# Kernel optimization log

Hardware: AMD Instinct MI355X
Metric: run time of the kernel (lower is better)

Reference implementation:

```python
import jax, jax.numpy as jnp
import numpy as np

Z, K, H, Y = 128, 256, 512, 4  # z_size, key_size, hidden_size, y_dim


def setup_inputs() -> dict:
    key = jax.random.key(0)
    ks = jax.random.split(key, 8)
    B, T, P = 512, 32, 32
    s = lambda k, shape, sc: (jax.random.normal(k, shape, jnp.float32) * sc)
    return {
        "x_seq": jax.random.normal(ks[0], (B, T, P, P), jnp.float32),
        "W_enc": s(ks[1], (P * P, Z), 0.03),
        "gamma": jnp.ones((Z,), jnp.float32),
        "beta": jnp.zeros((Z,), jnp.float32),
        "W_ih": s(ks[2], (4 * H, K + 1), 0.05),
        "W_hh": s(ks[3], (4 * H, H), 0.04),
        "b_ih": jnp.zeros((4 * H,), jnp.float32),
        "b_hh": jnp.zeros((4 * H,), jnp.float32),
        "W_key": s(ks[4], (K, H), 0.06),
        "b_key": jnp.zeros((K,), jnp.float32),
        "W_g": s(ks[5], (1, H), 0.06),
        "b_g": jnp.zeros((1,), jnp.float32),
        "conf_gain": jnp.ones((1,), jnp.float32),
        "conf_bias": jnp.zeros((1,), jnp.float32),
        "W_y": s(ks[6], (Y, H), 0.06),
        "b_y": jnp.zeros((Y,), jnp.float32),
    }


def _lstm_cell(x, h, c, W_ih, W_hh, b_ih, b_hh):
    # PyTorch gate order: i, f, g, o
    gates = x @ W_ih.T + b_ih + h @ W_hh.T + b_hh
    i, f, g, o = jnp.split(gates, 4, axis=-1)
    c = jax.nn.sigmoid(f) * c + jax.nn.sigmoid(i) * jnp.tanh(g)
    h = jax.nn.sigmoid(o) * jnp.tanh(c)
    return h, c


def _forward(x_seq, W_enc, gamma, beta, W_ih, W_hh, b_ih, b_hh,
             W_key, b_key, W_g, b_g, conf_gain, conf_bias, W_y, b_y):
    B, T, P, _ = x_seq.shape
    # encoder: flatten -> linear to z_size (stand-in for Encoder_mlp)
    z = x_seq.reshape(B, T, P * P) @ W_enc  # [B, T, Z]
    # context norm over the sequence dim (single task segment)
    mu = z.mean(axis=1, keepdims=True)
    sig = jnp.sqrt(z.var(axis=1, keepdims=True) + 1e-8)
    z = (z - mu) / sig * gamma + beta

    M = T + 1  # T+1 steps; final step feeds a zero z_t
    z_pad = jnp.concatenate([z, jnp.zeros((B, 1, Z), z.dtype)], axis=1)  # [B, M, Z]

    h0 = jnp.zeros((B, H), z.dtype)
    c0 = jnp.zeros((B, H), z.dtype)
    kr0 = jnp.zeros((B, K + 1), z.dtype)
    Mk0 = jnp.zeros((B, M, K), z.dtype)
    Mv0 = jnp.zeros((B, M, Z), z.dtype)

    def step(carry, t):
        h, c, key_r, M_k, M_v = carry
        z_t = jax.lax.dynamic_index_in_dim(z_pad, t, axis=1, keepdims=False)  # [B, Z]
        h, c = _lstm_cell(key_r, h, c, W_ih, W_hh, b_ih, b_hh)
        key_w = jax.nn.relu(h @ W_key.T + b_key)          # [B, K]
        g = jax.nn.sigmoid(h @ W_g.T + b_g)               # [B, 1]
        y_lin = h @ W_y.T + b_y                            # [B, Y]
        # attention read over valid memory slots j < t
        scores = jnp.einsum('bz,bmz->bm', z_t, M_v)        # [B, M]
        valid = (jnp.arange(M) < t)[None, :]
        w_k = jax.nn.softmax(jnp.where(valid, scores, -1e9), axis=1)
        c_k = jax.nn.sigmoid(scores * conf_gain + conf_bias)
        kv = jnp.concatenate([M_k, c_k[..., None]], axis=2)  # [B, M, K+1]
        attn = g * jnp.einsum('bm,bmd->bd', w_k, kv)          # [B, K+1]
        key_r_new = jnp.where(t == 0, jnp.zeros_like(attn), attn)
        # append to memory at slot t
        M_k = jax.lax.dynamic_update_slice_in_dim(M_k, key_w[:, None, :], t, axis=1)
        M_v = jax.lax.dynamic_update_slice_in_dim(M_v, z_t[:, None, :], t, axis=1)
        return (h, c, key_r_new, M_k, M_v), y_lin

    _, ys = jax.lax.scan(step, (h0, c0, kr0, Mk0, Mv0), jnp.arange(M))
    return ys[-1]  # y_pred_linear from final step, [B, Y]


def reference(x_seq, W_enc, gamma, beta, W_ih, W_hh, b_ih, b_hh,
              W_key, b_key, W_g, b_g, conf_gain, conf_bias, W_y, b_y):
    y_pred_linear = _forward(x_seq, W_enc, gamma, beta, W_ih, W_hh, b_ih, b_hh,
                             W_key, b_key, W_g, b_g, conf_gain, conf_bias, W_y, b_y)
    y_pred = jnp.argmax(y_pred_linear, axis=1)
    return y_pred_linear, y_pred
```

## Files before the change

kernel.cpp:

```cpp
#include <hip/hip_runtime.h>
#include <math.h>

typedef unsigned short ushort;
typedef unsigned int uint;
typedef __bf16 bf16x8 __attribute__((ext_vector_type(8)));
typedef float f32x4 __attribute__((ext_vector_type(4)));

#define ZS    128
#define KS    256
#define HS    512
#define BATCH 512
#define TT    32
#define MM    33
#define NB    2304
#define KPAD  800
#define HOFF  272
#define LDA   800

static __device__ __forceinline__ float sigf(float x) { return 1.f / (1.f + expf(-x)); }

__global__ void prep_w(const float* __restrict__ W_ih, const float* __restrict__ W_hh,
                       const float* __restrict__ W_key, const float* __restrict__ b_ih,
                       const float* __restrict__ b_hh, const float* __restrict__ b_key,
                       const float* __restrict__ W_enc,
                       ushort* __restrict__ Whi, ushort* __restrict__ Wlo,
                       ushort* __restrict__ Behi, ushort* __restrict__ Belo,
                       float* __restrict__ biasN)
{
    int idx = blockIdx.x * 256 + threadIdx.x;
    if (idx < NB) {
        float bv;
        if (idx < 2048) { int j = idx >> 2, gi = idx & 3, r = gi * 512 + j; bv = b_ih[r] + b_hh[r]; }
        else bv = b_key[idx - 2048];
        biasN[idx] = bv;
    }
    if (idx < NB * KPAD) {
        int n = idx / KPAD, k = idx - n * KPAD;
        float v = 0.f;
        if (n < 2048) {
            int j = n >> 2, gi = n & 3, r = gi * 512 + j;
            if (k < 257) v = W_ih[r * 257 + k];
            else if (k >= HOFF && k < HOFF + 512) v = W_hh[r * 512 + (k - HOFF)];
        } else {
            if (k >= HOFF && k < HOFF + 512) v = W_key[(n - 2048) * 512 + (k - HOFF)];
        }
        uint u = __float_as_uint(v);
        Whi[idx] = (ushort)(u >> 16);
        float lo = v - __uint_as_float(u & 0xFFFF0000u);
        Wlo[idx] = (ushort)(__float_as_uint(lo) >> 16);
    } else if (idx < NB * KPAD + 128 * 1024) {
        int e = idx - NB * KPAD;
        int n = e >> 10, k = e & 1023;
        float v = W_enc[k * 128 + n];
        uint u = __float_as_uint(v);
        Behi[e] = (ushort)(u >> 16);
        float lo = v - __uint_as_float(u & 0xFFFF0000u);
        Belo[e] = (ushort)(__float_as_uint(lo) >> 16);
    }
}

template<int BN, int MODE>
__global__ __launch_bounds__(256)
void gemm_mfma(const float* __restrict__ A, int lda,
               const ushort* __restrict__ Bhi, const ushort* __restrict__ Blo, int ldb,
               int nslice,
               float* __restrict__ out, const float* __restrict__ biasN,
               float* __restrict__ cst, float* __restrict__ Mk, int step)
{
    constexpr int NI = BN / 32;
    constexpr int AHI = 0, ALO = 2560, BHI = 5120, BLO = 5120 + 40 * BN;
    constexpr int BUF = 5120 + 80 * BN;
    __shared__ ushort lds[2 * BUF];

    const int tid = threadIdx.x;
    const int bx = blockIdx.x, by = blockIdx.y;
    const int row0 = by * 64, n0 = bx * BN;
    const int l = tid & 63, w = tid >> 6, wm = w >> 1, wn = w & 1;
    const int lm = l & 15, kg = (l >> 4) << 3;

    f32x4 acc[2][NI];
    const f32x4 zero4 = {0.f, 0.f, 0.f, 0.f};
#pragma unroll
    for (int mi = 0; mi < 2; mi++)
#pragma unroll
        for (int ni = 0; ni < NI; ni++) acc[mi][ni] = zero4;

    float4 av[2];
    uint4 bhv[BN / 64], blv[BN / 64];

    auto LOADG = [&](int s) {
        const int k0 = s * 32;
#pragma unroll
        for (int i = 0; i < 2; i++) {
            int idx = tid + 256 * i, r = idx >> 3, c = (idx & 7) << 2;
            av[i] = *(const float4*)(A + (size_t)(row0 + r) * lda + k0 + c);
        }
#pragma unroll
        for (int i = 0; i < BN / 64; i++) {
            int idx = tid + 256 * i, r = idx >> 2, c = (idx & 3) << 3;
            bhv[i] = *(const uint4*)(Bhi + (size_t)(n0 + r) * ldb + k0 + c);
            blv[i] = *(const uint4*)(Blo + (size_t)(n0 + r) * ldb + k0 + c);
        }
    };
    auto STORE = [&](int buf) {
        ushort* L = lds + buf * BUF;
#pragma unroll
        for (int i = 0; i < 2; i++) {
            int idx = tid + 256 * i, r = idx >> 3, c = (idx & 7) << 2;
            uint u0 = __float_as_uint(av[i].x), u1 = __float_as_uint(av[i].y);
            uint u2 = __float_as_uint(av[i].z), u3 = __float_as_uint(av[i].w);
            uint hp0 = (u1 & 0xFFFF0000u) | (u0 >> 16);
            uint hp1 = (u3 & 0xFFFF0000u) | (u2 >> 16);
            float l0 = av[i].x - __uint_as_float(u0 & 0xFFFF0000u);
            float l1 = av[i].y - __uint_as_float(u1 & 0xFFFF0000u);
            float l2 = av[i].z - __uint_as_float(u2 & 0xFFFF0000u);
            float l3 = av[i].w - __uint_as_float(u3 & 0xFFFF0000u);
            uint lp0 = (__float_as_uint(l1) & 0xFFFF0000u) | (__float_as_uint(l0) >> 16);
            uint lp1 = (__float_as_uint(l3) & 0xFFFF0000u) | (__float_as_uint(l2) >> 16);
            *(uint2*)&L[AHI + r * 40 + c] = make_uint2(hp0, hp1);
            *(uint2*)&L[ALO + r * 40 + c] = make_uint2(lp0, lp1);
        }
#pragma unroll
        for (int i = 0; i < BN / 64; i++) {
            int idx = tid + 256 * i, r = idx >> 2, c = (idx & 3) << 3;
            *(uint4*)&L[BHI + r * 40 + c] = bhv[i];
            *(uint4*)&L[BLO + r * 40 + c] = blv[i];
        }
    };

    LOADG(0);
    STORE(0);
    for (int s = 0; s < nslice; s++) {
        if (s + 1 < nslice) LOADG(s + 1);
        __syncthreads();
        const ushort* L = lds + (s & 1) * BUF;
        bf16x8 ah[2], alv[2], bh[NI], bl[NI];
#pragma unroll
        for (int mi = 0; mi < 2; mi++) {
            int r = wm * 32 + mi * 16 + lm;
            ah[mi]  = *(const bf16x8*)&L[AHI + r * 40 + kg];
            alv[mi] = *(const bf16x8*)&L[ALO + r * 40 + kg];
        }
#pragma unroll
        for (int ni = 0; ni < NI; ni++) {
            int r = wn * (BN / 2) + ni * 16 + lm;
            bh[ni] = *(const bf16x8*)&L[BHI + r * 40 + kg];
            bl[ni] = *(const bf16x8*)&L[BLO + r * 40 + kg];
        }
#pragma unroll
        for (int mi = 0; mi < 2; mi++)
#pragma unroll
            for (int ni = 0; ni < NI; ni++) {
                acc[mi][ni] = __builtin_amdgcn_mfma_f32_16x16x32_bf16(ah[mi],  bh[ni], acc[mi][ni], 0, 0, 0);
                acc[mi][ni] = __builtin_amdgcn_mfma_f32_16x16x32_bf16(ah[mi],  bl[ni], acc[mi][ni], 0, 0, 0);
                acc[mi][ni] = __builtin_amdgcn_mfma_f32_16x16x32_bf16(alv[mi], bh[ni], acc[mi][ni], 0, 0, 0);
            }
        if (s + 1 < nslice) STORE((s + 1) & 1);
    }

    const int crow = (l >> 4) << 2;
    if (MODE == 0) {
#pragma unroll
        for (int mi = 0; mi < 2; mi++)
#pragma unroll
            for (int ni = 0; ni < NI; ni++)
#pragma unroll
                for (int r = 0; r < 4; r++) {
                    int m = row0 + wm * 32 + mi * 16 + crow + r;
                    int z = n0 + wn * (BN / 2) + ni * 16 + lm;
                    out[(size_t)(m >> 5) * (MM * ZS) + (m & 31) * ZS + z] = acc[mi][ni][r];
                }
    } else if (bx < 32) {
        __syncthreads();
        float* epi = (float*)lds;
        float* ew = epi + w * 1088;
#pragma unroll
        for (int mi = 0; mi < 2; mi++)
#pragma unroll
            for (int ni = 0; ni < NI; ni++)
#pragma unroll
                for (int r = 0; r < 4; r++) {
                    int ml = mi * 16 + crow + r, nl = ni * 16 + lm;
                    ew[ml * 34 + nl] = acc[mi][ni][r] + biasN[n0 + wn * 32 + nl];
                }
        __syncthreads();
        int bl_ = tid >> 2, ug = tid & 3;
        int b = row0 + bl_;
        int j0 = bx * 16 + ug * 4;
        float4 cold = *(float4*)&cst[(size_t)b * HS + j0];
        float cc[4] = {cold.x, cold.y, cold.z, cold.w};
        float hv[4];
#pragma unroll
        for (int i = 0; i < 4; i++) {
            int ul = ug * 4 + i;
            float p[4];
#pragma unroll
            for (int g = 0; g < 4; g++) {
                int nb = ul * 4 + g;
                p[g] = epi[((bl_ >> 5) * 2 + (nb >> 5)) * 1088 + (bl_ & 31) * 34 + (nb & 31)];
            }
            float ig = sigf(p[0]), fg = sigf(p[1]), gg = tanhf(p[2]), og = sigf(p[3]);
            float cn = fg * cc[i] + ig * gg;
            hv[i] = og * tanhf(cn);
            cc[i] = cn;
        }
        *(float4*)&cst[(size_t)b * HS + j0] = make_float4(cc[0], cc[1], cc[2], cc[3]);
        *(float4*)&out[(size_t)b * LDA + HOFF + j0] = make_float4(hv[0], hv[1], hv[2], hv[3]);
    } else if (step >= 1) {
#pragma unroll
        for (int mi = 0; mi < 2; mi++)
#pragma unroll
            for (int ni = 0; ni < NI; ni++)
#pragma unroll
                for (int r = 0; r < 4; r++) {
                    int b = row0 + wm * 32 + mi * 16 + crow + r;
                    int cg = n0 + wn * 32 + ni * 16 + lm;
                    float v = fmaxf(acc[mi][ni][r] + biasN[cg], 0.f);
                    Mk[((size_t)(step - 1) * BATCH + b) * KS + (cg - 2048)] = v;
                }
    }
}

__global__ void norm_k(float* __restrict__ z_pad, const float* __restrict__ gamma,
                       const float* __restrict__ beta)
{
    int b = blockIdx.x, zc = threadIdx.x;
    float* zb = z_pad + (size_t)b * (MM * ZS);
    float s = 0.f, s2 = 0.f;
    for (int t = 0; t < TT; t++) { float v = zb[t * ZS + zc]; s += v; s2 += v * v; }
    float mu = s * (1.f / 32.f);
    float var = s2 * (1.f / 32.f) - mu * mu;
    float rstd = 1.f / sqrtf(var + 1e-8f);
    float ga = gamma[zc], be = beta[zc];
    for (int t = 0; t < TT; t++) {
        float v = zb[t * ZS + zc];
        zb[t * ZS + zc] = (v - mu) * rstd * ga + be;
    }
    zb[TT * ZS + zc] = 0.f;
}

__global__ __launch_bounds__(256)
void scores_k(const float* __restrict__ z_pad, const float* __restrict__ cg_p,
              const float* __restrict__ cb_p, float* __restrict__ watt,
              float* __restrict__ wc)
{
    __shared__ float zs[MM * 129];
    int b = blockIdx.x, tid = threadIdx.x;
    const float* zb = z_pad + (size_t)b * (MM * ZS);
    for (int i = tid; i < MM * ZS; i += 256) {
        int m = i >> 7, k = i & 127;
        zs[m * 129 + k] = zb[i];
    }
    __syncthreads();
    float cg = cg_p[0], cb = cb_p[0];
    int wid = tid >> 6, lane = tid & 63;
    for (int t = 1 + wid; t <= 32; t += 4) {
        int m = lane;
        float s = -3.0e38f;
        if (m < t) {
            const float* zt = &zs[t * 129];
            const float* zm = &zs[m * 129];
            float acc = 0.f;
#pragma unroll 8
            for (int k = 0; k < ZS; k++) acc += zt[k] * zm[k];
            s = acc;
        }
        float mx = s;
        for (int off = 1; off < 64; off <<= 1) mx = fmaxf(mx, __shfl_xor(mx, off));
        float e = (m < t) ? expf(s - mx) : 0.f;
        float sum = e;
        for (int off = 1; off < 64; off <<= 1) sum += __shfl_xor(sum, off);
        float w = e / sum;
        if (m < t) watt[(b * MM + t) * MM + m] = w;
        float p = (m < t) ? w * sigf(s * cg + cb) : 0.f;
        for (int off = 1; off < 64; off <<= 1) p += __shfl_xor(p, off);
        if (lane == 0) wc[b * MM + t] = p;
    }
}

__global__ __launch_bounds__(256)
void post_k(float* __restrict__ inpN, const float* __restrict__ W_g,
            const float* __restrict__ b_g, const float* __restrict__ watt,
            const float* __restrict__ wc, const float* __restrict__ Mk, int t)
{
    __shared__ float red[256];
    __shared__ float wts[32];
    __shared__ float gsh;
    int b = blockIdx.x, tid = threadIdx.x;
    float* row = inpN + (size_t)b * LDA;
    float h1 = row[HOFF + tid], h2 = row[HOFF + 256 + tid];
    red[tid] = h1 * W_g[tid] + h2 * W_g[tid + 256];
    if (tid < t) wts[tid] = watt[(b * MM + t) * MM + tid];
    __syncthreads();
    for (int s = 128; s > 0; s >>= 1) {
        if (tid < s) red[tid] += red[tid + s];
        __syncthreads();
    }
    if (tid == 0) gsh = sigf(red[0] + b_g[0]);
    __syncthreads();
    float g = gsh;
    float acc = 0.f;
    for (int m = 0; m < t; m++)
        acc += wts[m] * Mk[((size_t)m * BATCH + b) * KS + tid];
    row[tid] = g * acc;
    if (tid == 0) row[256] = g * wc[b * MM + t];
}

__global__ void y_k(const float* __restrict__ inpN, const float* __restrict__ W_y,
                    const float* __restrict__ b_y, float* __restrict__ out)
{
    int b = blockIdx.x, lane = threadIdx.x;
    const float* h = inpN + (size_t)b * LDA + HOFF;
    float a0 = 0, a1 = 0, a2 = 0, a3 = 0;
    for (int r = 0; r < 8; r++) {
        int k = lane + r * 64;
        float hv = h[k];
        a0 += hv * W_y[k];
        a1 += hv * W_y[512 + k];
        a2 += hv * W_y[1024 + k];
        a3 += hv * W_y[1536 + k];
    }
    for (int off = 32; off > 0; off >>= 1) {
        a0 += __shfl_xor(a0, off);
        a1 += __shfl_xor(a1, off);
        a2 += __shfl_xor(a2, off);
        a3 += __shfl_xor(a3, off);
    }
    if (lane == 0) {
        float y0 = a0 + b_y[0], y1 = a1 + b_y[1], y2 = a2 + b_y[2], y3 = a3 + b_y[3];
        out[b * 4 + 0] = y0; out[b * 4 + 1] = y1; out[b * 4 + 2] = y2; out[b * 4 + 3] = y3;
        int best = 0; float bv = y0;
        if (y1 > bv) { bv = y1; best = 1; }
        if (y2 > bv) { bv = y2; best = 2; }
        if (y3 > bv) { bv = y3; best = 3; }
        out[2048 + b] = (float)best;
    }
}

extern "C" void kernel_launch(void* const* d_in, const int* in_sizes, int n_in,
                              void* d_out, int out_size, void* d_ws, size_t ws_size,
                              hipStream_t stream)
{
    const float* x_seq = (const float*)d_in[0];
    const float* W_enc = (const float*)d_in[1];
    const float* gamma = (const float*)d_in[2];
    const float* beta  = (const float*)d_in[3];
    const float* W_ih  = (const float*)d_in[4];
    const float* W_hh  = (const float*)d_in[5];
    const float* b_ih  = (const float*)d_in[6];
    const float* b_hh  = (const float*)d_in[7];
    const float* W_key = (const float*)d_in[8];
    const float* b_key = (const float*)d_in[9];
    const float* W_g   = (const float*)d_in[10];
    const float* b_g   = (const float*)d_in[11];
    const float* cgain = (const float*)d_in[12];
    const float* cbias = (const float*)d_in[13];
    const float* W_y   = (const float*)d_in[14];
    const float* b_y   = (const float*)d_in[15];

    float* ws    = (float*)d_ws;
    float* z_pad = ws;
    float* watt  = z_pad + 2162688;
    float* wcv   = watt + 557568;
    float* Mk    = wcv + 16896;
    float* inp0  = Mk + 4194304;
    float* inp1  = inp0 + 409600;
    float* cst   = inp1 + 409600;
    float* biasN = cst + 262144;
    ushort* Whi  = (ushort*)(biasN + 2304);
    ushort* Wlo  = Whi + NB * KPAD;
    ushort* Behi = Wlo + NB * KPAD;
    ushort* Belo = Behi + 131072;

    hipMemsetAsync(inp0, 0, (size_t)(409600 * 2 + 262144) * sizeof(float), stream);

    prep_w<<<(NB * KPAD + 131072 + 255) / 256, 256, 0, stream>>>(
        W_ih, W_hh, W_key, b_ih, b_hh, b_key, W_enc, Whi, Wlo, Behi, Belo, biasN);

    gemm_mfma<128, 0><<<dim3(1, 256), 256, 0, stream>>>(
        x_seq, 1024, Behi, Belo, 1024, 32, z_pad, nullptr, nullptr, nullptr, 0);
    norm_k<<<512, 128, 0, stream>>>(z_pad, gamma, beta);
    scores_k<<<512, 256, 0, stream>>>(z_pad, cgain, cbias, watt, wcv);

    for (int t = 0; t <= 32; t++) {
        float* inC = (t & 1) ? inp1 : inp0;
        float* inN = (t & 1) ? inp0 : inp1;
        gemm_mfma<64, 1><<<dim3(36, 8), 256, 0, stream>>>(
            inC, LDA, Whi, Wlo, KPAD, 25, inN, biasN, cst, Mk, t);
        if (t >= 1 && t <= 31)
            post_k<<<512, 256, 0, stream>>>(inN, W_g, b_g, watt, wcv, Mk, t);
    }
    y_k<<<512, 64, 0, stream>>>(inp1, W_y, b_y, (float*)d_out);
}
```

Measured before the change: 1.140 ms.

## Halve GEMM row tile and store recurrent activations pre-split as bf16 hi/lo

The GEMM row tile shrinks from 64 to 32 rows and a min-blocks launch bound is added, doubling the grid of the per-step LSTM GEMM (36x16) and the encoder GEMM (1x512) so more CUs are occupied. The recurrent input buffers are now stored as pre-split bf16 hi/lo pairs, written by the GEMM epilogue and post_k, so the per-step GEMM loads ready-made bf16 A tiles and skips the fp32 split arithmetic in its staging path. This trades more reloading of B tiles across row blocks and an extra split in the epilogues for less per-step A conversion and better parallelism.

```diff
diff --git a/kernel.cpp b/kernel.cpp
--- a/kernel.cpp
+++ b/kernel.cpp
@@ -18,6 +18,7 @@
 #define LDA   800
 
 static __device__ __forceinline__ float sigf(float x) { return 1.f / (1.f + expf(-x)); }
+static __device__ __forceinline__ float bf2f(ushort u) { return __uint_as_float((uint)u << 16); }
 
 __global__ void prep_w(const float* __restrict__ W_ih, const float* __restrict__ W_hh,
                        const float* __restrict__ W_key, const float* __restrict__ b_ih,
@@ -59,41 +60,46 @@
     }
 }
 
-template<int BN, int MODE>
-__global__ __launch_bounds__(256)
-void gemm_mfma(const float* __restrict__ A, int lda,
+template<int BN, int MODE, bool PRESPLIT>
+__global__ __launch_bounds__(256, 4)
+void gemm_mfma(const float* __restrict__ A,
+               const ushort* __restrict__ Ahi, const ushort* __restrict__ Alo, int lda,
                const ushort* __restrict__ Bhi, const ushort* __restrict__ Blo, int ldb,
                int nslice,
-               float* __restrict__ out, const float* __restrict__ biasN,
+               float* __restrict__ out,
+               ushort* __restrict__ outHi, ushort* __restrict__ outLo,
+               const float* __restrict__ biasN,
                float* __restrict__ cst, float* __restrict__ Mk, int step)
 {
     constexpr int NI = BN / 32;
-    constexpr int AHI = 0, ALO = 2560, BHI = 5120, BLO = 5120 + 40 * BN;
-    constexpr int BUF = 5120 + 80 * BN;
+    constexpr int AHI = 0, ALO = 32 * 40, BHI = 64 * 40, BLO = 64 * 40 + BN * 40;
+    constexpr int BUF = 64 * 40 + 2 * BN * 40;
     __shared__ ushort lds[2 * BUF];
 
     const int tid = threadIdx.x;
     const int bx = blockIdx.x, by = blockIdx.y;
-    const int row0 = by * 64, n0 = bx * BN;
+    const int row0 = by * 32, n0 = bx * BN;
     const int l = tid & 63, w = tid >> 6, wm = w >> 1, wn = w & 1;
     const int lm = l & 15, kg = (l >> 4) << 3;
 
-    f32x4 acc[2][NI];
+    f32x4 acc[NI];
     const f32x4 zero4 = {0.f, 0.f, 0.f, 0.f};
 #pragma unroll
-    for (int mi = 0; mi < 2; mi++)
-#pragma unroll
-        for (int ni = 0; ni < NI; ni++) acc[mi][ni] = zero4;
-
-    float4 av[2];
+    for (int ni = 0; ni < NI; ni++) acc[ni] = zero4;
+
+    float4 avf;
+    uint4 avu;
     uint4 bhv[BN / 64], blv[BN / 64];
 
     auto LOADG = [&](int s) {
         const int k0 = s * 32;
-#pragma unroll
-        for (int i = 0; i < 2; i++) {
-            int idx = tid + 256 * i, r = idx >> 3, c = (idx & 7) << 2;
-            av[i] = *(const float4*)(A + (size_t)(row0 + r) * lda + k0 + c);
+        if (PRESPLIT) {
+            int idx = tid & 127, r = idx >> 2, c = (idx & 3) << 3;
+            const ushort* src = (tid < 128) ? Ahi : Alo;
+            avu = *(const uint4*)(src + (size_t)(row0 + r) * lda + k0 + c);
+        } else {
+            int r = tid >> 3, c = (tid & 7) << 2;
+            avf = *(const float4*)(A + (size_t)(row0 + r) * lda + k0 + c);
         }
 #pragma unroll
         for (int i = 0; i < BN / 64; i++) {
@@ -104,17 +110,19 @@
     };
     auto STORE = [&](int buf) {
         ushort* L = lds + buf * BUF;
-#pragma unroll
-        for (int i = 0; i < 2; i++) {
-            int idx = tid + 256 * i, r = idx >> 3, c = (idx & 7) << 2;
-            uint u0 = __float_as_uint(av[i].x), u1 = __float_as_uint(av[i].y);
-            uint u2 = __float_as_uint(av[i].z), u3 = __float_as_uint(av[i].w);
+        if (PRESPLIT) {
+            int idx = tid & 127, r = idx >> 2, c = (idx & 3) << 3;
+            *(uint4*)&L[(tid < 128 ? AHI : ALO) + r * 40 + c] = avu;
+        } else {
+            int r = tid >> 3, c = (tid & 7) << 2;
+            uint u0 = __float_as_uint(avf.x), u1 = __float_as_uint(avf.y);
+            uint u2 = __float_as_uint(avf.z), u3 = __float_as_uint(avf.w);
             uint hp0 = (u1 & 0xFFFF0000u) | (u0 >> 16);
             uint hp1 = (u3 & 0xFFFF0000u) | (u2 >> 16);
-            float l0 = av[i].x - __uint_as_float(u0 & 0xFFFF0000u);
-            float l1 = av[i].y - __uint_as_float(u1 & 0xFFFF0000u);
-            float l2 = av[i].z - __uint_as_float(u2 & 0xFFFF0000u);
-            float l3 = av[i].w - __uint_as_float(u3 & 0xFFFF0000u);
+            float l0 = avf.x - __uint_as_float(u0 & 0xFFFF0000u);
+            float l1 = avf.y - __uint_as_float(u1 & 0xFFFF0000u);
+            float l2 = avf.z - __uint_as_float(u2 & 0xFFFF0000u);
+            float l3 = avf.w - __uint_as_float(u3 & 0xFFFF0000u);
             uint lp0 = (__float_as_uint(l1) & 0xFFFF0000u) | (__float_as_uint(l0) >> 16);
             uint lp1 = (__float_as_uint(l3) & 0xFFFF0000u) | (__float_as_uint(l2) >> 16);
             *(uint2*)&L[AHI + r * 40 + c] = make_uint2(hp0, hp1);
@@ -134,12 +142,11 @@
         if (s + 1 < nslice) LOADG(s + 1);
         __syncthreads();
         const ushort* L = lds + (s & 1) * BUF;
-        bf16x8 ah[2], alv[2], bh[NI], bl[NI];
-#pragma unroll
-        for (int mi = 0; mi < 2; mi++) {
-            int r = wm * 32 + mi * 16 + lm;
-            ah[mi]  = *(const bf16x8*)&L[AHI + r * 40 + kg];
-            alv[mi] = *(const bf16x8*)&L[ALO + r * 40 + kg];
+        bf16x8 ah, alv, bh[NI], bl[NI];
+        {
+            int r = wm * 16 + lm;
+            ah  = *(const bf16x8*)&L[AHI + r * 40 + kg];
+            alv = *(const bf16x8*)&L[ALO + r * 40 + kg];
         }
 #pragma unroll
         for (int ni = 0; ni < NI; ni++) {
@@ -148,76 +155,74 @@
             bl[ni] = *(const bf16x8*)&L[BLO + r * 40 + kg];
         }
 #pragma unroll
-        for (int mi = 0; mi < 2; mi++)
-#pragma unroll
-            for (int ni = 0; ni < NI; ni++) {
-                acc[mi][ni] = __builtin_amdgcn_mfma_f32_16x16x32_bf16(ah[mi],  bh[ni], acc[mi][ni], 0, 0, 0);
-                acc[mi][ni] = __builtin_amdgcn_mfma_f32_16x16x32_bf16(ah[mi],  bl[ni], acc[mi][ni], 0, 0, 0);
-                acc[mi][ni] = __builtin_amdgcn_mfma_f32_16x16x32_bf16(alv[mi], bh[ni], acc[mi][ni], 0, 0, 0);
-            }
+        for (int ni = 0; ni < NI; ni++) {
+            acc[ni] = __builtin_amdgcn_mfma_f32_16x16x32_bf16(ah,  bh[ni], acc[ni], 0, 0, 0);
+            acc[ni] = __builtin_amdgcn_mfma_f32_16x16x32_bf16(ah,  bl[ni], acc[ni], 0, 0, 0);
+            acc[ni] = __builtin_amdgcn_mfma_f32_16x16x32_bf16(alv, bh[ni], acc[ni], 0, 0, 0);
+        }
         if (s + 1 < nslice) STORE((s + 1) & 1);
     }
 
     const int crow = (l >> 4) << 2;
     if (MODE == 0) {
 #pragma unroll
-        for (int mi = 0; mi < 2; mi++)
-#pragma unroll
-            for (int ni = 0; ni < NI; ni++)
-#pragma unroll
-                for (int r = 0; r < 4; r++) {
-                    int m = row0 + wm * 32 + mi * 16 + crow + r;
-                    int z = n0 + wn * (BN / 2) + ni * 16 + lm;
-                    out[(size_t)(m >> 5) * (MM * ZS) + (m & 31) * ZS + z] = acc[mi][ni][r];
-                }
+        for (int ni = 0; ni < NI; ni++)
+#pragma unroll
+            for (int r = 0; r < 4; r++) {
+                int m = row0 + wm * 16 + crow + r;
+                int z = n0 + wn * (BN / 2) + ni * 16 + lm;
+                out[(size_t)(m >> 5) * (MM * ZS) + (m & 31) * ZS + z] = acc[ni][r];
+            }
     } else if (bx < 32) {
         __syncthreads();
         float* epi = (float*)lds;
-        float* ew = epi + w * 1088;
-#pragma unroll
-        for (int mi = 0; mi < 2; mi++)
-#pragma unroll
-            for (int ni = 0; ni < NI; ni++)
-#pragma unroll
-                for (int r = 0; r < 4; r++) {
-                    int ml = mi * 16 + crow + r, nl = ni * 16 + lm;
-                    ew[ml * 34 + nl] = acc[mi][ni][r] + biasN[n0 + wn * 32 + nl];
-                }
+        float* ew = epi + w * 544;
+#pragma unroll
+        for (int ni = 0; ni < NI; ni++)
+#pragma unroll
+            for (int r = 0; r < 4; r++) {
+                int ml = crow + r, nl = ni * 16 + lm;
+                ew[ml * 34 + nl] = acc[ni][r] + biasN[n0 + wn * 32 + nl];
+            }
         __syncthreads();
-        int bl_ = tid >> 2, ug = tid & 3;
-        int b = row0 + bl_;
-        int j0 = bx * 16 + ug * 4;
-        float4 cold = *(float4*)&cst[(size_t)b * HS + j0];
-        float cc[4] = {cold.x, cold.y, cold.z, cold.w};
-        float hv[4];
-#pragma unroll
-        for (int i = 0; i < 4; i++) {
-            int ul = ug * 4 + i;
+        int row = tid >> 3, jj8 = tid & 7;
+        int b = row0 + row;
+        int j0 = bx * 16 + jj8 * 2;
+        float2 cold = *(float2*)&cst[(size_t)b * HS + j0];
+        float cc[2] = {cold.x, cold.y}, hv[2];
+#pragma unroll
+        for (int i = 0; i < 2; i++) {
+            int jj = jj8 * 2 + i;
             float p[4];
 #pragma unroll
             for (int g = 0; g < 4; g++) {
-                int nb = ul * 4 + g;
-                p[g] = epi[((bl_ >> 5) * 2 + (nb >> 5)) * 1088 + (bl_ & 31) * 34 + (nb & 31)];
+                int n = jj * 4 + g;
+                int wv = (row >> 4) * 2 + (n >> 5);
+                p[g] = epi[wv * 544 + (row & 15) * 34 + (n & 31)];
             }
             float ig = sigf(p[0]), fg = sigf(p[1]), gg = tanhf(p[2]), og = sigf(p[3]);
             float cn = fg * cc[i] + ig * gg;
             hv[i] = og * tanhf(cn);
             cc[i] = cn;
         }
-        *(float4*)&cst[(size_t)b * HS + j0] = make_float4(cc[0], cc[1], cc[2], cc[3]);
-        *(float4*)&out[(size_t)b * LDA + HOFF + j0] = make_float4(hv[0], hv[1], hv[2], hv[3]);
+        *(float2*)&cst[(size_t)b * HS + j0] = make_float2(cc[0], cc[1]);
+        uint u0 = __float_as_uint(hv[0]), u1 = __float_as_uint(hv[1]);
+        uint hp = (u1 & 0xFFFF0000u) | (u0 >> 16);
+        float l0 = hv[0] - __uint_as_float(u0 & 0xFFFF0000u);
+        float l1 = hv[1] - __uint_as_float(u1 & 0xFFFF0000u);
+        uint lp = (__float_as_uint(l1) & 0xFFFF0000u) | (__float_as_uint(l0) >> 16);
+        *(uint*)&outHi[(size_t)b * LDA + HOFF + j0] = hp;
+        *(uint*)&outLo[(size_t)b * LDA + HOFF + j0] = lp;
     } else if (step >= 1) {
 #pragma unroll
-        for (int mi = 0; mi < 2; mi++)
-#pragma unroll
-            for (int ni = 0; ni < NI; ni++)
-#pragma unroll
-                for (int r = 0; r < 4; r++) {
-                    int b = row0 + wm * 32 + mi * 16 + crow + r;
-                    int cg = n0 + wn * 32 + ni * 16 + lm;
-                    float v = fmaxf(acc[mi][ni][r] + biasN[cg], 0.f);
-                    Mk[((size_t)(step - 1) * BATCH + b) * KS + (cg - 2048)] = v;
-                }
+        for (int ni = 0; ni < NI; ni++)
+#pragma unroll
+            for (int r = 0; r < 4; r++) {
+                int b = row0 + wm * 16 + crow + r;
+                int cg = n0 + wn * 32 + ni * 16 + lm;
+                float v = fmaxf(acc[ni][r] + biasN[cg], 0.f);
+                Mk[((size_t)(step - 1) * BATCH + b) * KS + (cg - 2048)] = v;
+            }
     }
 }
 
@@ -279,16 +284,19 @@
 }
 
 __global__ __launch_bounds__(256)
-void post_k(float* __restrict__ inpN, const float* __restrict__ W_g,
-            const float* __restrict__ b_g, const float* __restrict__ watt,
-            const float* __restrict__ wc, const float* __restrict__ Mk, int t)
+void post_k(ushort* __restrict__ inpHi, ushort* __restrict__ inpLo,
+            const float* __restrict__ W_g, const float* __restrict__ b_g,
+            const float* __restrict__ watt, const float* __restrict__ wc,
+            const float* __restrict__ Mk, int t)
 {
     __shared__ float red[256];
     __shared__ float wts[32];
     __shared__ float gsh;
     int b = blockIdx.x, tid = threadIdx.x;
-    float* row = inpN + (size_t)b * LDA;
-    float h1 = row[HOFF + tid], h2 = row[HOFF + 256 + tid];
+    ushort* rHi = inpHi + (size_t)b * LDA;
+    ushort* rLo = inpLo + (size_t)b * LDA;
+    float h1 = bf2f(rHi[HOFF + tid]) + bf2f(rLo[HOFF + tid]);
+    float h2 = bf2f(rHi[HOFF + 256 + tid]) + bf2f(rLo[HOFF + 256 + tid]);
     red[tid] = h1 * W_g[tid] + h2 * W_g[tid + 256];
     if (tid < t) wts[tid] = watt[(b * MM + t) * MM + tid];
     __syncthreads();
@@ -302,19 +310,31 @@
     float acc = 0.f;
     for (int m = 0; m < t; m++)
         acc += wts[m] * Mk[((size_t)m * BATCH + b) * KS + tid];
-    row[tid] = g * acc;
-    if (tid == 0) row[256] = g * wc[b * MM + t];
-}
-
-__global__ void y_k(const float* __restrict__ inpN, const float* __restrict__ W_y,
-                    const float* __restrict__ b_y, float* __restrict__ out)
+    float v = g * acc;
+    uint u = __float_as_uint(v);
+    rHi[tid] = (ushort)(u >> 16);
+    float lo = v - __uint_as_float(u & 0xFFFF0000u);
+    rLo[tid] = (ushort)(__float_as_uint(lo) >> 16);
+    if (tid == 0) {
+        float vc = g * wc[b * MM + t];
+        uint uc = __float_as_uint(vc);
+        rHi[256] = (ushort)(uc >> 16);
+        float lc = vc - __uint_as_float(uc & 0xFFFF0000u);
+        rLo[256] = (ushort)(__float_as_uint(lc) >> 16);
+    }
+}
+
+__global__ void y_k(const ushort* __restrict__ inpHi, const ushort* __restrict__ inpLo,
+                    const float* __restrict__ W_y, const float* __restrict__ b_y,
+                    float* __restrict__ out)
 {
     int b = blockIdx.x, lane = threadIdx.x;
-    const float* h = inpN + (size_t)b * LDA + HOFF;
+    const ushort* hHi = inpHi + (size_t)b * LDA + HOFF;
+    const ushort* hLo = inpLo + (size_t)b * LDA + HOFF;
     float a0 = 0, a1 = 0, a2 = 0, a3 = 0;
     for (int r = 0; r < 8; r++) {
         int k = lane + r * 64;
-        float hv = h[k];
+        float hv = bf2f(hHi[k]) + bf2f(hLo[k]);
         a0 += hv * W_y[k];
         a1 += hv * W_y[512 + k];
         a2 += hv * W_y[1024 + k];
@@ -363,32 +383,39 @@
     float* watt  = z_pad + 2162688;
     float* wcv   = watt + 557568;
     float* Mk    = wcv + 16896;
-    float* inp0  = Mk + 4194304;
-    float* inp1  = inp0 + 409600;
-    float* cst   = inp1 + 409600;
-    float* biasN = cst + 262144;
-    ushort* Whi  = (ushort*)(biasN + 2304);
+    float* biasN = Mk + 4194304;
+    float* cst   = biasN + 2304;
+    ushort* inpHi0 = (ushort*)(cst + 262144);
+    ushort* inpLo0 = inpHi0 + 409600;
+    ushort* inpHi1 = inpLo0 + 409600;
+    ushort* inpLo1 = inpHi1 + 409600;
+    ushort* Whi  = inpLo1 + 409600;
     ushort* Wlo  = Whi + NB * KPAD;
     ushort* Behi = Wlo + NB * KPAD;
     ushort* Belo = Behi + 131072;
 
-    hipMemsetAsync(inp0, 0, (size_t)(409600 * 2 + 262144) * sizeof(float), stream);
+    hipMemsetAsync(cst, 0, 262144 * sizeof(float) + 4 * 409600 * sizeof(ushort), stream);
 
     prep_w<<<(NB * KPAD + 131072 + 255) / 256, 256, 0, stream>>>(
         W_ih, W_hh, W_key, b_ih, b_hh, b_key, W_enc, Whi, Wlo, Behi, Belo, biasN);
 
-    gemm_mfma<128, 0><<<dim3(1, 256), 256, 0, stream>>>(
-        x_seq, 1024, Behi, Belo, 1024, 32, z_pad, nullptr, nullptr, nullptr, 0);
+    gemm_mfma<128, 0, false><<<dim3(1, 512), 256, 0, stream>>>(
+        x_seq, nullptr, nullptr, 1024, Behi, Belo, 1024, 32,
+        z_pad, nullptr, nullptr, nullptr, nullptr, nullptr, 0);
     norm_k<<<512, 128, 0, stream>>>(z_pad, gamma, beta);
     scores_k<<<512, 256, 0, stream>>>(z_pad, cgain, cbias, watt, wcv);
 
     for (int t = 0; t <= 32; t++) {
-        float* inC = (t & 1) ? inp1 : inp0;
-        float* inN = (t & 1) ? inp0 : inp1;
-        gemm_mfma<64, 1><<<dim3(36, 8), 256, 0, stream>>>(
-            inC, LDA, Whi, Wlo, KPAD, 25, inN, biasN, cst, Mk, t);
+        ushort* inHiC = (t & 1) ? inpHi1 : inpHi0;
+        ushort* inLoC = (t & 1) ? inpLo1 : inpLo0;
+        ushort* inHiN = (t & 1) ? inpHi0 : inpHi1;
+        ushort* inLoN = (t & 1) ? inpLo0 : inpLo1;
+        gemm_mfma<64, 1, true><<<dim3(36, 16), 256, 0, stream>>>(
+            nullptr, inHiC, inLoC, LDA, Whi, Wlo, KPAD, 25,
+            nullptr, inHiN, inLoN, biasN, cst, Mk, t);
         if (t >= 1 && t <= 31)
-            post_k<<<512, 256, 0, stream>>>(inN, W_g, b_g, watt, wcv, Mk, t);
-    }
-    y_k<<<512, 64, 0, stream>>>(inp1, W_y, b_y, (float*)d_out);
-}
+            post_k<<<512, 256, 0, stream>>>(inHiN, inLoN, W_g, b_g, watt, wcv, Mk, t);
+    }
+    y_k<<<512, 64, 0, stream>>>((0 ? inpHi0 : inpHi1), (0 ? inpLo0 : inpLo1),
+                                W_y, b_y, (float*)d_out);
+}
```

Result: faster. 1.015 ms (-11.0%).
